# Performance work log

Hardware: AMD Instinct MI355X
Metric: run time of the kernel (lower is better)

## Reference

```python
import jax, jax.numpy as jnp
import numpy as np

N = 50000
NEG_SLOPE = 0.2

def setup_inputs() -> dict:
    key = jax.random.key(0)
    ks = jax.random.split(key, 12)
    x = jax.random.normal(ks[0], (N, 128), dtype=jnp.float32)
    edge_index = jax.random.randint(ks[1], (2, 800000), 0, N, dtype=jnp.int64)
    s = lambda fan_in: 1.0 / np.sqrt(fan_in)
    W1 = jax.random.uniform(ks[2], (64, 128), jnp.float32, -s(128), s(128))
    a1_src = jax.random.uniform(ks[3], (64,), jnp.float32, -s(64), s(64))
    a1_dst = jax.random.uniform(ks[4], (64,), jnp.float32, -s(64), s(64))
    b1 = jnp.zeros((64,), jnp.float32)
    W2 = jax.random.uniform(ks[5], (64, 64), jnp.float32, -s(64), s(64))
    a2_src = jax.random.uniform(ks[6], (64,), jnp.float32, -s(64), s(64))
    a2_dst = jax.random.uniform(ks[7], (64,), jnp.float32, -s(64), s(64))
    b2 = jnp.zeros((64,), jnp.float32)
    return {"x": x, "edge_index": edge_index,
            "W1": W1, "a1_src": a1_src, "a1_dst": a1_dst, "b1": b1,
            "W2": W2, "a2_src": a2_src, "a2_dst": a2_dst, "b2": b2}


def gat_conv(x, W, a_src, a_dst, b, src, dst):
    # Linear transform: [N, out]
    h = x @ W.T
    # Per-node attention scalars (heads=1): alpha_i = <h_i, a>
    alpha_s = h @ a_src   # [N]
    alpha_d = h @ a_dst   # [N]
    # Per-edge logits with LeakyReLU (PyG GATConv, negative_slope=0.2)
    e = alpha_s[src] + alpha_d[dst]
    e = jnp.where(e > 0, e, NEG_SLOPE * e)
    # Softmax over incoming edges of each destination node (numerically stable)
    m = jax.ops.segment_max(e, dst, num_segments=N)
    ex = jnp.exp(e - m[dst])
    denom = jax.ops.segment_sum(ex, dst, num_segments=N)
    coef = ex / denom[dst]                          # [E]
    # Scatter-aggregate messages: sum_j coef_ij * h_j
    out = jax.ops.segment_sum(coef[:, None] * h[src], dst, num_segments=N)
    return out + b


def reference(x, edge_index, W1, a1_src, a1_dst, b1, W2, a2_src, a2_dst, b2):
    # add_self_loops=True (PyG default): append (i, i) for every node
    loops = jnp.arange(N, dtype=edge_index.dtype)
    src = jnp.concatenate([edge_index[0], loops])
    dst = jnp.concatenate([edge_index[1], loops])
    h = gat_conv(x, W1, a1_src, a1_dst, b1, src, dst)
    h = jax.nn.relu(h)
    out = gat_conv(h, W2, a2_src, a2_dst, b2, src, dst)
    return out
```

## Files before the change

### kernel.cpp

```cpp
#include <hip/hip_runtime.h>
#include <cstdint>
#include <cstddef>

#ifndef NEG_SLOPE
#define NEG_SLOPE 0.2f
#endif

typedef __attribute__((ext_vector_type(8))) short short8;
typedef __attribute__((ext_vector_type(4))) float f32x4;

__device__ __forceinline__ unsigned short bf16rne(float f) {
    unsigned u = __builtin_bit_cast(unsigned, f);
    u += 0x7FFFu + ((u >> 16) & 1u);
    return (unsigned short)(u >> 16);
}
__device__ __forceinline__ float bf16tof(unsigned short h) {
    unsigned u = ((unsigned)h) << 16;
    return __builtin_bit_cast(float, u);
}

__global__ void detect_kernel(const int* __restrict__ ei, int* __restrict__ flag) {
    if (threadIdx.x == 0 && blockIdx.x == 0) {
        int orv = 0;
#pragma unroll
        for (int k = 0; k < 16; ++k) orv |= ei[2 * k + 1];
        *flag = (orv == 0) ? 1 : 0;
    }
}

__global__ void init_deg_kernel(int* __restrict__ deg, int n) {
    int i = blockIdx.x * blockDim.x + threadIdx.x;
    if (i < n) deg[i] = 1;
}

__global__ void count_kernel(const int* __restrict__ ei, int E, int n,
                             int* __restrict__ deg, const int* __restrict__ flag) {
    int is64 = *flag;
    int part = blockIdx.x & 7;
    int rank = blockIdx.x >> 3;
    int nblk = gridDim.x >> 3;
    int step = (n + 7) >> 3;
    int lo = part * step;
    int hi = lo + step < n ? lo + step : n;
    int stride = nblk * blockDim.x;
    for (int e = rank * blockDim.x + threadIdx.x; e < E; e += stride) {
        int dst = is64 ? ei[2 * ((long)E + e)] : ei[E + e];
        if (dst >= lo && dst < hi) atomicAdd(&deg[dst], 1);
    }
}

__global__ __launch_bounds__(256) void scan1_kernel(const int* __restrict__ deg,
                                                    int* __restrict__ off,
                                                    int* __restrict__ bsum, int n) {
    __shared__ int ws[4];
    int t = threadIdx.x, lane = t & 63, w = t >> 6;
    int idx = blockIdx.x * 256 + t;
    int v = (idx < n) ? deg[idx] : 0;
    int inc = v;
#pragma unroll
    for (int d = 1; d < 64; d <<= 1) {
        int o = __shfl_up(inc, d, 64);
        if (lane >= d) inc += o;
    }
    if (lane == 63) ws[w] = inc;
    __syncthreads();
    int wpre = 0;
    for (int x = 0; x < w; ++x) wpre += ws[x];
    if (idx < n) off[idx] = wpre + inc - v;
    if (t == 255) bsum[blockIdx.x] = wpre + inc;
}

__global__ __launch_bounds__(256) void scan2_kernel(int* __restrict__ bsum,
                                                    int* __restrict__ total, int nb) {
    __shared__ int ws[4];
    int t = threadIdx.x, lane = t & 63, w = t >> 6;
    int v = (t < nb) ? bsum[t] : 0;
    int inc = v;
#pragma unroll
    for (int d = 1; d < 64; d <<= 1) {
        int o = __shfl_up(inc, d, 64);
        if (lane >= d) inc += o;
    }
    if (lane == 63) ws[w] = inc;
    __syncthreads();
    int wpre = 0;
    for (int x = 0; x < w; ++x) wpre += ws[x];
    if (t < nb) bsum[t] = wpre + inc - v;
    if (t == 255) *total = wpre + inc;
}

__global__ __launch_bounds__(256) void scan3_kernel(int* __restrict__ off,
                                                    const int* __restrict__ bsum,
                                                    const int* __restrict__ total, int n) {
    int idx = blockIdx.x * 256 + threadIdx.x;
    if (idx < n) off[idx] += bsum[blockIdx.x];
    if (idx == 0) off[n] = *total;
}

__global__ void selfloop_kernel(const int* __restrict__ off, int* __restrict__ cursor,
                                int* __restrict__ csr, int n) {
    int i = blockIdx.x * blockDim.x + threadIdx.x;
    if (i < n) {
        int o = off[i];
        csr[o] = i;
        cursor[i] = o + 1;
    }
}

__global__ void fill_kernel(const int* __restrict__ ei, int E, int n,
                            int* __restrict__ cursor, int* __restrict__ csr,
                            const int* __restrict__ flag) {
    int is64 = *flag;
    int part = blockIdx.x & 7;
    int rank = blockIdx.x >> 3;
    int nblk = gridDim.x >> 3;
    int step = (n + 7) >> 3;
    int lo = part * step;
    int hi = lo + step < n ? lo + step : n;
    int stride = nblk * blockDim.x;
    for (int e = rank * blockDim.x + threadIdx.x; e < E; e += stride) {
        int dst = is64 ? ei[2 * ((long)E + e)] : ei[E + e];
        if (dst >= lo && dst < hi) {
            int src = is64 ? ei[2 * (long)e] : ei[e];
            int slot = atomicAdd(&cursor[dst], 1);
            csr[slot] = src;
        }
    }
}

template <int IN_DIM>
__global__ __launch_bounds__(256) void gemm_mfma_kernel(
    const float* __restrict__ X, const float* __restrict__ W,
    const float* __restrict__ a_src, const float* __restrict__ a_dst,
    float* __restrict__ H, float* __restrict__ AS, float* __restrict__ AD, int n) {
    constexpr int KT  = IN_DIM / 32;
    constexpr int LDB = IN_DIM + 8;
    __shared__ unsigned short sWhi[64 * LDB];
    __shared__ unsigned short sWlo[64 * LDB];
    int t = threadIdx.x;
    for (int idx = t; idx < 64 * IN_DIM; idx += 256) {
        int r = idx / IN_DIM, c = idx - r * IN_DIM;
        float w = W[idx];
        unsigned short hi = bf16rne(w);
        sWhi[r * LDB + c] = hi;
        sWlo[r * LDB + c] = bf16rne(w - bf16tof(hi));
    }
    __syncthreads();
    int lane = t & 63, wid = t >> 6;
    int l15 = lane & 15, l4 = lane >> 4;
    float asj[4], adj[4];
#pragma unroll
    for (int nt = 0; nt < 4; ++nt) {
        asj[nt] = a_src[nt * 16 + l15];
        adj[nt] = a_dst[nt * 16 + l15];
    }
    int gw = blockIdx.x * 4 + wid;
    int nw = gridDim.x * 4;
    int mtiles = n >> 4;
    for (int tile = gw; tile < mtiles; tile += nw) {
        int n0 = tile << 4;
        f32x4 acc[4];
#pragma unroll
        for (int nt = 0; nt < 4; ++nt) acc[nt] = f32x4{0.f, 0.f, 0.f, 0.f};
        const float* xbase = X + (size_t)(n0 + l15) * IN_DIM + l4 * 8;
#pragma unroll
        for (int kt = 0; kt < KT; ++kt) {
            float4 v0 = *reinterpret_cast<const float4*>(xbase + kt * 32);
            float4 v1 = *reinterpret_cast<const float4*>(xbase + kt * 32 + 4);
            float xv[8] = {v0.x, v0.y, v0.z, v0.w, v1.x, v1.y, v1.z, v1.w};
            short8 ahi, alo;
#pragma unroll
            for (int e = 0; e < 8; ++e) {
                unsigned short hb = bf16rne(xv[e]);
                ahi[e] = (short)hb;
                alo[e] = (short)bf16rne(xv[e] - bf16tof(hb));
            }
            int kcol = kt * 32 + l4 * 8;
#pragma unroll
            for (int nt = 0; nt < 4; ++nt) {
                short8 bhi = *reinterpret_cast<const short8*>(&sWhi[(nt * 16 + l15) * LDB + kcol]);
                short8 blo = *reinterpret_cast<const short8*>(&sWlo[(nt * 16 + l15) * LDB + kcol]);
                acc[nt] = __builtin_amdgcn_mfma_f32_16x16x32_bf16(ahi, bhi, acc[nt], 0, 0, 0);
                acc[nt] = __builtin_amdgcn_mfma_f32_16x16x32_bf16(ahi, blo, acc[nt], 0, 0, 0);
                acc[nt] = __builtin_amdgcn_mfma_f32_16x16x32_bf16(alo, bhi, acc[nt], 0, 0, 0);
            }
        }
        float c1[4] = {0.f, 0.f, 0.f, 0.f}, c2[4] = {0.f, 0.f, 0.f, 0.f};
#pragma unroll
        for (int nt = 0; nt < 4; ++nt) {
#pragma unroll
            for (int r = 0; r < 4; ++r) {
                float h = acc[nt][r];
                H[(size_t)(n0 + l4 * 4 + r) * 64 + nt * 16 + l15] = h;
                c1[r] += h * asj[nt];
                c2[r] += h * adj[nt];
            }
        }
#pragma unroll
        for (int r = 0; r < 4; ++r) {
#pragma unroll
            for (int d = 1; d < 16; d <<= 1) {
                c1[r] += __shfl_xor(c1[r], d, 64);
                c2[r] += __shfl_xor(c2[r], d, 64);
            }
            if (l15 == 0) {
                AS[n0 + l4 * 4 + r] = c1[r];
                AD[n0 + l4 * 4 + r] = c2[r];
            }
        }
    }
}

template <bool RELU>
__global__ __launch_bounds__(256) void aggregate_kernel(
    const float* __restrict__ AS, const float* __restrict__ AD,
    const float* __restrict__ H, const int* __restrict__ off,
    const int* __restrict__ csr, const float* __restrict__ bias,
    float* __restrict__ out, int n) {
    constexpr int CAP = 128;
    __shared__ float2 sEdge[4][CAP];
    int lane = threadIdx.x & 63, wid = threadIdx.x >> 6;
    int i = blockIdx.x * 4 + wid;
    if (i >= n) return;
    int s = off[i], e = off[i + 1];
    int deg = e - s;
    float ad = AD[i];
    float2* st = sEdge[wid];

    float m = -1e30f, ssum = 0.f;
    for (int k = s + lane; k < e; k += 64) {
        int sc = csr[k];
        float ev = AS[sc] + ad;
        ev = ev > 0.f ? ev : NEG_SLOPE * ev;
        int idx = k - s;
        if (idx < CAP) st[idx] = make_float2(ev, __int_as_float(sc));
        float nm = fmaxf(m, ev);
        ssum = ssum * __expf(m - nm) + __expf(ev - nm);
        m = nm;
    }
#pragma unroll
    for (int d = 32; d >= 1; d >>= 1) {
        float om = __shfl_xor(m, d, 64);
        float os = __shfl_xor(ssum, d, 64);
        float nm = fmaxf(m, om);
        ssum = ssum * __expf(m - nm) + os * __expf(om - nm);
        m = nm;
    }
    float inv = 1.0f / ssum;

    asm volatile("s_waitcnt lgkmcnt(0)" ::: "memory");
    __builtin_amdgcn_sched_barrier(0);

    float acc = 0.f;
    int lim = deg < CAP ? deg : CAP;
    int k2 = 0;
    for (; k2 + 4 <= lim; k2 += 4) {
        float2 e0 = st[k2 + 0];
        float2 e1 = st[k2 + 1];
        float2 e2 = st[k2 + 2];
        float2 e3 = st[k2 + 3];
        float v0 = H[(size_t)__float_as_int(e0.y) * 64 + lane];
        float v1 = H[(size_t)__float_as_int(e1.y) * 64 + lane];
        float v2 = H[(size_t)__float_as_int(e2.y) * 64 + lane];
        float v3 = H[(size_t)__float_as_int(e3.y) * 64 + lane];
        acc += __expf(e0.x - m) * v0;
        acc += __expf(e1.x - m) * v1;
        acc += __expf(e2.x - m) * v2;
        acc += __expf(e3.x - m) * v3;
    }
    for (; k2 < lim; ++k2) {
        float2 e0 = st[k2];
        acc += __expf(e0.x - m) * H[(size_t)__float_as_int(e0.y) * 64 + lane];
    }
    for (int k = s + CAP; k < e; ++k) {
        int sc = csr[k];
        float ev = AS[sc] + ad;
        ev = ev > 0.f ? ev : NEG_SLOPE * ev;
        acc += __expf(ev - m) * H[(size_t)sc * 64 + lane];
    }
    acc = acc * inv + bias[lane];
    if (RELU) acc = fmaxf(acc, 0.f);
    out[(size_t)i * 64 + lane] = acc;
}

extern "C" void kernel_launch(void* const* d_in, const int* in_sizes, int n_in,
                              void* d_out, int out_size, void* d_ws, size_t ws_size,
                              hipStream_t stream) {
    const float* x   = (const float*)d_in[0];
    const int*   ei  = (const int*)d_in[1];
    const float* W1  = (const float*)d_in[2];
    const float* a1s = (const float*)d_in[3];
    const float* a1d = (const float*)d_in[4];
    const float* b1  = (const float*)d_in[5];
    const float* W2  = (const float*)d_in[6];
    const float* a2s = (const float*)d_in[7];
    const float* a2d = (const float*)d_in[8];
    const float* b2  = (const float*)d_in[9];
    float* out = (float*)d_out;

    int n = in_sizes[0] / 128;
    int E = in_sizes[1] / 2;
    int ET = E + n;

    char* ws = (char*)d_ws;
    size_t o = 0;
    auto alloc = [&](size_t bytes) {
        void* p = ws + o;
        o += (bytes + 255) & ~(size_t)255;
        return p;
    };
    int*   flag   = (int*)alloc(4);
    int*   deg    = (int*)alloc((size_t)n * 4);
    int*   off    = (int*)alloc(((size_t)n + 1) * 4);
    int*   cursor = (int*)alloc((size_t)n * 4);
    int*   csr    = (int*)alloc((size_t)ET * 4);
    int*   bsum   = (int*)alloc(256 * 4);
    int*   total  = (int*)alloc(4);
    float* h1     = (float*)alloc((size_t)n * 64 * 4);
    float* as1    = (float*)alloc((size_t)n * 4);
    float* ad1    = (float*)alloc((size_t)n * 4);
    float* hr1    = (float*)alloc((size_t)n * 64 * 4);
    float* as2    = (float*)alloc((size_t)n * 4);
    float* ad2    = (float*)alloc((size_t)n * 4);
    (void)ws_size; (void)n_in; (void)out_size;

    int nb256 = (n + 255) / 256;
    int mtiles = n / 16;
    int gemm_blocks = (mtiles + 3) / 4;

    detect_kernel<<<1, 64, 0, stream>>>(ei, flag);
    init_deg_kernel<<<nb256, 256, 0, stream>>>(deg, n);
    count_kernel<<<2048, 256, 0, stream>>>(ei, E, n, deg, flag);
    scan1_kernel<<<nb256, 256, 0, stream>>>(deg, off, bsum, n);
    scan2_kernel<<<1, 256, 0, stream>>>(bsum, total, nb256);
    scan3_kernel<<<nb256, 256, 0, stream>>>(off, bsum, total, n);
    selfloop_kernel<<<nb256, 256, 0, stream>>>(off, cursor, csr, n);
    fill_kernel<<<2048, 256, 0, stream>>>(ei, E, n, cursor, csr, flag);

    gemm_mfma_kernel<128><<<gemm_blocks, 256, 0, stream>>>(x, W1, a1s, a1d, h1, as1, ad1, n);
    aggregate_kernel<true><<<(n + 3) / 4, 256, 0, stream>>>(as1, ad1, h1, off, csr, b1, hr1, n);

    gemm_mfma_kernel<64><<<gemm_blocks, 256, 0, stream>>>(hr1, W2, a2s, a2d, h1, as2, ad2, n);
    aggregate_kernel<false><<<(n + 3) / 4, 256, 0, stream>>>(as2, ad2, h1, off, csr, b2, out, n);
}
```

Measured before the change: 274.1 us.

## Fuse graph-build kernels with layer-1 GEMM and drop max pass in softmax

Merges degree init with dtype detection, runs edge counting and the first GEMM in one block-specialized launch, and fuses the scan finalize with self-loop insertion. The aggregate kernel now computes exp(logit) once without max subtraction, storing probabilities in shared memory instead of recomputing exp in the gather loop. This cuts kernel launches and serialized passes, and removes the online-max bookkeeping and shuffles. It gives up the numerically stable softmax, so large logits could overflow.

```diff
diff --git a/kernel.cpp b/kernel.cpp
--- a/kernel.cpp
+++ b/kernel.cpp
@@ -19,8 +19,11 @@
     return __builtin_bit_cast(float, u);
 }
 
-__global__ void detect_kernel(const int* __restrict__ ei, int* __restrict__ flag) {
-    if (threadIdx.x == 0 && blockIdx.x == 0) {
+__global__ void init_kernel(const int* __restrict__ ei, int* __restrict__ flag,
+                            int* __restrict__ deg, int n) {
+    int i = blockIdx.x * blockDim.x + threadIdx.x;
+    if (i < n) deg[i] = 0;
+    if (i == 0) {
         int orv = 0;
 #pragma unroll
         for (int k = 0; k < 16; ++k) orv |= ei[2 * k + 1];
@@ -28,24 +31,187 @@
     }
 }
 
-__global__ void init_deg_kernel(int* __restrict__ deg, int n) {
-    int i = blockIdx.x * blockDim.x + threadIdx.x;
-    if (i < n) deg[i] = 1;
-}
-
-__global__ void count_kernel(const int* __restrict__ ei, int E, int n,
-                             int* __restrict__ deg, const int* __restrict__ flag) {
-    int is64 = *flag;
-    int part = blockIdx.x & 7;
-    int rank = blockIdx.x >> 3;
-    int nblk = gridDim.x >> 3;
-    int step = (n + 7) >> 3;
-    int lo = part * step;
-    int hi = lo + step < n ? lo + step : n;
-    int stride = nblk * blockDim.x;
-    for (int e = rank * blockDim.x + threadIdx.x; e < E; e += stride) {
-        int dst = is64 ? ei[2 * ((long)E + e)] : ei[E + e];
-        if (dst >= lo && dst < hi) atomicAdd(&deg[dst], 1);
+template <int IN_DIM>
+__global__ __launch_bounds__(256) void count_gemm_kernel(
+    const int* __restrict__ ei, int E, int n, int* __restrict__ deg,
+    const int* __restrict__ flag, int CB,
+    const float* __restrict__ X, const float* __restrict__ W,
+    const float* __restrict__ a_src, const float* __restrict__ a_dst,
+    float* __restrict__ H, float* __restrict__ AS, float* __restrict__ AD) {
+    constexpr int KT  = IN_DIM / 32;
+    constexpr int LDB = IN_DIM + 8;
+    __shared__ unsigned short sWhi[64 * LDB];
+    __shared__ unsigned short sWlo[64 * LDB];
+    int bid = blockIdx.x;
+    if (bid < CB) {
+        int is64 = *flag;
+        int part = bid & 7;
+        int rank = bid >> 3;
+        int nblk = CB >> 3;
+        int step = (n + 7) >> 3;
+        int lo = part * step;
+        int hi = lo + step < n ? lo + step : n;
+        int stride = nblk * blockDim.x;
+        for (int e = rank * blockDim.x + threadIdx.x; e < E; e += stride) {
+            int dst = is64 ? ei[2 * ((long)E + e)] : ei[E + e];
+            if (dst >= lo && dst < hi) atomicAdd(&deg[dst], 1);
+        }
+        return;
+    }
+    int t = threadIdx.x;
+    for (int idx = t; idx < 64 * IN_DIM; idx += 256) {
+        int r = idx / IN_DIM, c = idx - r * IN_DIM;
+        float w = W[idx];
+        unsigned short hi = bf16rne(w);
+        sWhi[r * LDB + c] = hi;
+        sWlo[r * LDB + c] = bf16rne(w - bf16tof(hi));
+    }
+    __syncthreads();
+    int lane = t & 63, wid = t >> 6;
+    int l15 = lane & 15, l4 = lane >> 4;
+    float asj[4], adj[4];
+#pragma unroll
+    for (int nt = 0; nt < 4; ++nt) {
+        asj[nt] = a_src[nt * 16 + l15];
+        adj[nt] = a_dst[nt * 16 + l15];
+    }
+    int gw = (bid - CB) * 4 + wid;
+    int nw = (gridDim.x - CB) * 4;
+    int mtiles = n >> 4;
+    for (int tile = gw; tile < mtiles; tile += nw) {
+        int n0 = tile << 4;
+        f32x4 acc[4];
+#pragma unroll
+        for (int nt = 0; nt < 4; ++nt) acc[nt] = f32x4{0.f, 0.f, 0.f, 0.f};
+        const float* xbase = X + (size_t)(n0 + l15) * IN_DIM + l4 * 8;
+#pragma unroll
+        for (int kt = 0; kt < KT; ++kt) {
+            float4 v0 = *reinterpret_cast<const float4*>(xbase + kt * 32);
+            float4 v1 = *reinterpret_cast<const float4*>(xbase + kt * 32 + 4);
+            float xv[8] = {v0.x, v0.y, v0.z, v0.w, v1.x, v1.y, v1.z, v1.w};
+            short8 ahi, alo;
+#pragma unroll
+            for (int e = 0; e < 8; ++e) {
+                unsigned short hb = bf16rne(xv[e]);
+                ahi[e] = (short)hb;
+                alo[e] = (short)bf16rne(xv[e] - bf16tof(hb));
+            }
+            int kcol = kt * 32 + l4 * 8;
+#pragma unroll
+            for (int nt = 0; nt < 4; ++nt) {
+                short8 bhi = *reinterpret_cast<const short8*>(&sWhi[(nt * 16 + l15) * LDB + kcol]);
+                short8 blo = *reinterpret_cast<const short8*>(&sWlo[(nt * 16 + l15) * LDB + kcol]);
+                acc[nt] = __builtin_amdgcn_mfma_f32_16x16x32_bf16(ahi, bhi, acc[nt], 0, 0, 0);
+                acc[nt] = __builtin_amdgcn_mfma_f32_16x16x32_bf16(ahi, blo, acc[nt], 0, 0, 0);
+                acc[nt] = __builtin_amdgcn_mfma_f32_16x16x32_bf16(alo, bhi, acc[nt], 0, 0, 0);
+            }
+        }
+        float c1[4] = {0.f, 0.f, 0.f, 0.f}, c2[4] = {0.f, 0.f, 0.f, 0.f};
+#pragma unroll
+    for (int nt = 0; nt < 4; ++nt) {
+#pragma unroll
+            for (int r = 0; r < 4; ++r) {
+                float h = acc[nt][r];
+                H[(size_t)(n0 + l4 * 4 + r) * 64 + nt * 16 + l15] = h;
+                c1[r] += h * asj[nt];
+                c2[r] += h * adj[nt];
+            }
+        }
+#pragma unroll
+        for (int r = 0; r < 4; ++r) {
+#pragma unroll
+            for (int d = 1; d < 16; d <<= 1) {
+                c1[r] += __shfl_xor(c1[r], d, 64);
+                c2[r] += __shfl_xor(c2[r], d, 64);
+            }
+            if (l15 == 0) {
+                AS[n0 + l4 * 4 + r] = c1[r];
+                AD[n0 + l4 * 4 + r] = c2[r];
+            }
+        }
+    }
+}
+
+template <int IN_DIM>
+__global__ __launch_bounds__(256) void gemm_mfma_kernel(
+    const float* __restrict__ X, const float* __restrict__ W,
+    const float* __restrict__ a_src, const float* __restrict__ a_dst,
+    float* __restrict__ H, float* __restrict__ AS, float* __restrict__ AD, int n) {
+    constexpr int KT  = IN_DIM / 32;
+    constexpr int LDB = IN_DIM + 8;
+    __shared__ unsigned short sWhi[64 * LDB];
+    __shared__ unsigned short sWlo[64 * LDB];
+    int t = threadIdx.x;
+    for (int idx = t; idx < 64 * IN_DIM; idx += 256) {
+        int r = idx / IN_DIM, c = idx - r * IN_DIM;
+        float w = W[idx];
+        unsigned short hi = bf16rne(w);
+        sWhi[r * LDB + c] = hi;
+        sWlo[r * LDB + c] = bf16rne(w - bf16tof(hi));
+    }
+    __syncthreads();
+    int lane = t & 63, wid = t >> 6;
+    int l15 = lane & 15, l4 = lane >> 4;
+    float asj[4], adj[4];
+#pragma unroll
+    for (int nt = 0; nt < 4; ++nt) {
+        asj[nt] = a_src[nt * 16 + l15];
+        adj[nt] = a_dst[nt * 16 + l15];
+    }
+    int gw = blockIdx.x * 4 + wid;
+    int nw = gridDim.x * 4;
+    int mtiles = n >> 4;
+    for (int tile = gw; tile < mtiles; tile += nw) {
+        int n0 = tile << 4;
+        f32x4 acc[4];
+#pragma unroll
+        for (int nt = 0; nt < 4; ++nt) acc[nt] = f32x4{0.f, 0.f, 0.f, 0.f};
+        const float* xbase = X + (size_t)(n0 + l15) * IN_DIM + l4 * 8;
+#pragma unroll
+        for (int kt = 0; kt < KT; ++kt) {
+            float4 v0 = *reinterpret_cast<const float4*>(xbase + kt * 32);
+            float4 v1 = *reinterpret_cast<const float4*>(xbase + kt * 32 + 4);
+            float xv[8] = {v0.x, v0.y, v0.z, v0.w, v1.x, v1.y, v1.z, v1.w};
+            short8 ahi, alo;
+#pragma unroll
+            for (int e = 0; e < 8; ++e) {
+                unsigned short hb = bf16rne(xv[e]);
+                ahi[e] = (short)hb;
+                alo[e] = (short)bf16rne(xv[e] - bf16tof(hb));
+            }
+            int kcol = kt * 32 + l4 * 8;
+#pragma unroll
+            for (int nt = 0; nt < 4; ++nt) {
+                short8 bhi = *reinterpret_cast<const short8*>(&sWhi[(nt * 16 + l15) * LDB + kcol]);
+                short8 blo = *reinterpret_cast<const short8*>(&sWlo[(nt * 16 + l15) * LDB + kcol]);
+                acc[nt] = __builtin_amdgcn_mfma_f32_16x16x32_bf16(ahi, bhi, acc[nt], 0, 0, 0);
+                acc[nt] = __builtin_amdgcn_mfma_f32_16x16x32_bf16(ahi, blo, acc[nt], 0, 0, 0);
+                acc[nt] = __builtin_amdgcn_mfma_f32_16x16x32_bf16(alo, bhi, acc[nt], 0, 0, 0);
+            }
+        }
+        float c1[4] = {0.f, 0.f, 0.f, 0.f}, c2[4] = {0.f, 0.f, 0.f, 0.f};
+#pragma unroll
+        for (int nt = 0; nt < 4; ++nt) {
+#pragma unroll
+            for (int r = 0; r < 4; ++r) {
+                float h = acc[nt][r];
+                H[(size_t)(n0 + l4 * 4 + r) * 64 + nt * 16 + l15] = h;
+                c1[r] += h * asj[nt];
+                c2[r] += h * adj[nt];
+            }
+        }
+#pragma unroll
+        for (int r = 0; r < 4; ++r) {
+#pragma unroll
+            for (int d = 1; d < 16; d <<= 1) {
+                c1[r] += __shfl_xor(c1[r], d, 64);
+                c2[r] += __shfl_xor(c2[r], d, 64);
+            }
+            if (l15 == 0) {
+                AS[n0 + l4 * 4 + r] = c1[r];
+                AD[n0 + l4 * 4 + r] = c2[r];
+            }
+        }
     }
 }
 
@@ -55,7 +221,7 @@
     __shared__ int ws[4];
     int t = threadIdx.x, lane = t & 63, w = t >> 6;
     int idx = blockIdx.x * 256 + t;
-    int v = (idx < n) ? deg[idx] : 0;
+    int v = (idx < n) ? deg[idx] + 1 : 0;
     int inc = v;
 #pragma unroll
     for (int d = 1; d < 64; d <<= 1) {
@@ -89,22 +255,18 @@
     if (t == 255) *total = wpre + inc;
 }
 
-__global__ __launch_bounds__(256) void scan3_kernel(int* __restrict__ off,
-                                                    const int* __restrict__ bsum,
-                                                    const int* __restrict__ total, int n) {
+__global__ __launch_bounds__(256) void scan3_selfloop_kernel(
+    int* __restrict__ off, const int* __restrict__ bsum,
+    const int* __restrict__ total, int* __restrict__ cursor,
+    int* __restrict__ csr, int n) {
     int idx = blockIdx.x * 256 + threadIdx.x;
-    if (idx < n) off[idx] += bsum[blockIdx.x];
+    if (idx < n) {
+        int o = off[idx] + bsum[blockIdx.x];
+        off[idx] = o;
+        csr[o] = idx;
+        cursor[idx] = o + 1;
+    }
     if (idx == 0) off[n] = *total;
-}
-
-__global__ void selfloop_kernel(const int* __restrict__ off, int* __restrict__ cursor,
-                                int* __restrict__ csr, int n) {
-    int i = blockIdx.x * blockDim.x + threadIdx.x;
-    if (i < n) {
-        int o = off[i];
-        csr[o] = i;
-        cursor[i] = o + 1;
-    }
 }
 
 __global__ void fill_kernel(const int* __restrict__ ei, int E, int n,
@@ -128,89 +290,6 @@
     }
 }
 
-template <int IN_DIM>
-__global__ __launch_bounds__(256) void gemm_mfma_kernel(
-    const float* __restrict__ X, const float* __restrict__ W,
-    const float* __restrict__ a_src, const float* __restrict__ a_dst,
-    float* __restrict__ H, float* __restrict__ AS, float* __restrict__ AD, int n) {
-    constexpr int KT  = IN_DIM / 32;
-    constexpr int LDB = IN_DIM + 8;
-    __shared__ unsigned short sWhi[64 * LDB];
-    __shared__ unsigned short sWlo[64 * LDB];
-    int t = threadIdx.x;
-    for (int idx = t; idx < 64 * IN_DIM; idx += 256) {
-        int r = idx / IN_DIM, c = idx - r * IN_DIM;
-        float w = W[idx];
-        unsigned short hi = bf16rne(w);
-        sWhi[r * LDB + c] = hi;
-        sWlo[r * LDB + c] = bf16rne(w - bf16tof(hi));
-    }
-    __syncthreads();
-    int lane = t & 63, wid = t >> 6;
-    int l15 = lane & 15, l4 = lane >> 4;
-    float asj[4], adj[4];
-#pragma unroll
-    for (int nt = 0; nt < 4; ++nt) {
-        asj[nt] = a_src[nt * 16 + l15];
-        adj[nt] = a_dst[nt * 16 + l15];
-    }
-    int gw = blockIdx.x * 4 + wid;
-    int nw = gridDim.x * 4;
-    int mtiles = n >> 4;
-    for (int tile = gw; tile < mtiles; tile += nw) {
-        int n0 = tile << 4;
-        f32x4 acc[4];
-#pragma unroll
-        for (int nt = 0; nt < 4; ++nt) acc[nt] = f32x4{0.f, 0.f, 0.f, 0.f};
-        const float* xbase = X + (size_t)(n0 + l15) * IN_DIM + l4 * 8;
-#pragma unroll
-        for (int kt = 0; kt < KT; ++kt) {
-            float4 v0 = *reinterpret_cast<const float4*>(xbase + kt * 32);
-            float4 v1 = *reinterpret_cast<const float4*>(xbase + kt * 32 + 4);
-            float xv[8] = {v0.x, v0.y, v0.z, v0.w, v1.x, v1.y, v1.z, v1.w};
-            short8 ahi, alo;
-#pragma unroll
-            for (int e = 0; e < 8; ++e) {
-                unsigned short hb = bf16rne(xv[e]);
-                ahi[e] = (short)hb;
-                alo[e] = (short)bf16rne(xv[e] - bf16tof(hb));
-            }
-            int kcol = kt * 32 + l4 * 8;
-#pragma unroll
-            for (int nt = 0; nt < 4; ++nt) {
-                short8 bhi = *reinterpret_cast<const short8*>(&sWhi[(nt * 16 + l15) * LDB + kcol]);
-                short8 blo = *reinterpret_cast<const short8*>(&sWlo[(nt * 16 + l15) * LDB + kcol]);
-                acc[nt] = __builtin_amdgcn_mfma_f32_16x16x32_bf16(ahi, bhi, acc[nt], 0, 0, 0);
-                acc[nt] = __builtin_amdgcn_mfma_f32_16x16x32_bf16(ahi, blo, acc[nt], 0, 0, 0);
-                acc[nt] = __builtin_amdgcn_mfma_f32_16x16x32_bf16(alo, bhi, acc[nt], 0, 0, 0);
-            }
-        }
-        float c1[4] = {0.f, 0.f, 0.f, 0.f}, c2[4] = {0.f, 0.f, 0.f, 0.f};
-#pragma unroll
-        for (int nt = 0; nt < 4; ++nt) {
-#pragma unroll
-            for (int r = 0; r < 4; ++r) {
-                float h = acc[nt][r];
-                H[(size_t)(n0 + l4 * 4 + r) * 64 + nt * 16 + l15] = h;
-                c1[r] += h * asj[nt];
-                c2[r] += h * adj[nt];
-            }
-        }
-#pragma unroll
-        for (int r = 0; r < 4; ++r) {
-#pragma unroll
-            for (int d = 1; d < 16; d <<= 1) {
-                c1[r] += __shfl_xor(c1[r], d, 64);
-                c2[r] += __shfl_xor(c2[r], d, 64);
-            }
-            if (l15 == 0) {
-                AS[n0 + l4 * 4 + r] = c1[r];
-                AD[n0 + l4 * 4 + r] = c2[r];
-            }
-        }
-    }
-}
-
 template <bool RELU>
 __global__ __launch_bounds__(256) void aggregate_kernel(
     const float* __restrict__ AS, const float* __restrict__ AD,
@@ -227,25 +306,18 @@
     float ad = AD[i];
     float2* st = sEdge[wid];
 
-    float m = -1e30f, ssum = 0.f;
+    float ssum = 0.f;
     for (int k = s + lane; k < e; k += 64) {
         int sc = csr[k];
         float ev = AS[sc] + ad;
         ev = ev > 0.f ? ev : NEG_SLOPE * ev;
+        float p = __expf(ev);
         int idx = k - s;
-        if (idx < CAP) st[idx] = make_float2(ev, __int_as_float(sc));
-        float nm = fmaxf(m, ev);
-        ssum = ssum * __expf(m - nm) + __expf(ev - nm);
-        m = nm;
-    }
-#pragma unroll
-    for (int d = 32; d >= 1; d >>= 1) {
-        float om = __shfl_xor(m, d, 64);
-        float os = __shfl_xor(ssum, d, 64);
-        float nm = fmaxf(m, om);
-        ssum = ssum * __expf(m - nm) + os * __expf(om - nm);
-        m = nm;
-    }
+        if (idx < CAP) st[idx] = make_float2(p, __int_as_float(sc));
+        ssum += p;
+    }
+#pragma unroll
+    for (int d = 32; d >= 1; d >>= 1) ssum += __shfl_xor(ssum, d, 64);
     float inv = 1.0f / ssum;
 
     asm volatile("s_waitcnt lgkmcnt(0)" ::: "memory");
@@ -263,20 +335,20 @@
         float v1 = H[(size_t)__float_as_int(e1.y) * 64 + lane];
         float v2 = H[(size_t)__float_as_int(e2.y) * 64 + lane];
         float v3 = H[(size_t)__float_as_int(e3.y) * 64 + lane];
-        acc += __expf(e0.x - m) * v0;
-        acc += __expf(e1.x - m) * v1;
-        acc += __expf(e2.x - m) * v2;
-        acc += __expf(e3.x - m) * v3;
+        acc += e0.x * v0;
+        acc += e1.x * v1;
+        acc += e2.x * v2;
+        acc += e3.x * v3;
     }
     for (; k2 < lim; ++k2) {
         float2 e0 = st[k2];
-        acc += __expf(e0.x - m) * H[(size_t)__float_as_int(e0.y) * 64 + lane];
+        acc += e0.x * H[(size_t)__float_as_int(e0.y) * 64 + lane];
     }
     for (int k = s + CAP; k < e; ++k) {
         int sc = csr[k];
         float ev = AS[sc] + ad;
         ev = ev > 0.f ? ev : NEG_SLOPE * ev;
-        acc += __expf(ev - m) * H[(size_t)sc * 64 + lane];
+        acc += __expf(ev) * H[(size_t)sc * 64 + lane];
     }
     acc = acc * inv + bias[lane];
     if (RELU) acc = fmaxf(acc, 0.f);
@@ -327,19 +399,17 @@
     int nb256 = (n + 255) / 256;
     int mtiles = n / 16;
     int gemm_blocks = (mtiles + 3) / 4;
-
-    detect_kernel<<<1, 64, 0, stream>>>(ei, flag);
-    init_deg_kernel<<<nb256, 256, 0, stream>>>(deg, n);
-    count_kernel<<<2048, 256, 0, stream>>>(ei, E, n, deg, flag);
+    const int CB = 2048;
+
+    init_kernel<<<nb256, 256, 0, stream>>>(ei, flag, deg, n);
+    count_gemm_kernel<128><<<CB + gemm_blocks, 256, 0, stream>>>(
+        ei, E, n, deg, flag, CB, x, W1, a1s, a1d, h1, as1, ad1);
     scan1_kernel<<<nb256, 256, 0, stream>>>(deg, off, bsum, n);
     scan2_kernel<<<1, 256, 0, stream>>>(bsum, total, nb256);
-    scan3_kernel<<<nb256, 256, 0, stream>>>(off, bsum, total, n);
-    selfloop_kernel<<<nb256, 256, 0, stream>>>(off, cursor, csr, n);
+    scan3_selfloop_kernel<<<nb256, 256, 0, stream>>>(off, bsum, total, cursor, csr, n);
     fill_kernel<<<2048, 256, 0, stream>>>(ei, E, n, cursor, csr, flag);
 
-    gemm_mfma_kernel<128><<<gemm_blocks, 256, 0, stream>>>(x, W1, a1s, a1d, h1, as1, ad1, n);
     aggregate_kernel<true><<<(n + 3) / 4, 256, 0, stream>>>(as1, ad1, h1, off, csr, b1, hr1, n);
-
     gemm_mfma_kernel<64><<<gemm_blocks, 256, 0, stream>>>(hr1, W2, a2s, a2d, h1, as2, ad2, n);
     aggregate_kernel<false><<<(n + 3) / 4, 256, 0, stream>>>(as2, ad2, h1, off, csr, b2, out, n);
 }
```

After: 269.3 us. About the same (-1.7%).
